# Kernel optimization log

Hardware: AMD Instinct MI355X
Metric: run time of the kernel (lower is better)

The kernel has to match this reference:

```python
import jax, jax.numpy as jnp
import numpy as np

DIM, DEPTH, HEADS, DHEAD, FF = 768, 6, 12, 64, 3072


def layer_norm(x, g, b, eps=1e-5):
    m = jnp.mean(x, axis=-1, keepdims=True)
    v = jnp.mean((x - m) ** 2, axis=-1, keepdims=True)
    return (x - m) * jax.lax.rsqrt(v + eps) * g + b


def setup_inputs() -> dict:
    key = jax.random.key(0)
    ks = jax.random.split(key, 8)
    s = 0.02
    inp = {
        "x": jax.random.normal(ks[0], (2, 2048, DIM), jnp.float32),
        "mask": jnp.ones((2, 2048), dtype=bool),
        "ln1_g": jnp.ones((DEPTH, DIM)), "ln1_b": jnp.zeros((DEPTH, DIM)),
        "w_qkv": jax.random.normal(ks[1], (DEPTH, DIM, 3 * HEADS * DHEAD)) * s,
        "w_out": jax.random.normal(ks[2], (DEPTH, HEADS * DHEAD, DIM)) * s,
        "b_out": jnp.zeros((DEPTH, DIM)),
        "ln2_g": jnp.ones((DEPTH, DIM)), "ln2_b": jnp.zeros((DEPTH, DIM)),
        "w_ff1": jax.random.normal(ks[3], (DEPTH, DIM, FF)) * s,
        "b_ff1": jnp.zeros((DEPTH, FF)),
        "w_ff2": jax.random.normal(ks[4], (DEPTH, FF, DIM)) * s,
        "b_ff2": jnp.zeros((DEPTH, DIM)),
        "lnf_g": jnp.ones((DIM,)), "lnf_b": jnp.zeros((DIM,)),
    }
    return inp


def reference(x, mask, ln1_g, ln1_b, w_qkv, w_out, b_out, ln2_g, ln2_b,
              w_ff1, b_ff1, w_ff2, b_ff2, lnf_g, lnf_b):
    scale = DHEAD ** -0.5
    b, n, _ = x.shape
    neg = -jnp.finfo(x.dtype).max
    mask4 = mask[:, None, None, :]  # b 1 1 j
    for l in range(DEPTH):
        # --- attention (pre-norm) ---
        h = layer_norm(x, ln1_g[l], ln1_b[l])
        qkv = h @ w_qkv[l]                           # [b, n, 3*h*d]
        q, k, v = jnp.split(qkv, 3, axis=-1)
        q = q.reshape(b, n, HEADS, DHEAD).transpose(0, 2, 1, 3)
        k = k.reshape(b, n, HEADS, DHEAD).transpose(0, 2, 1, 3)
        v = v.reshape(b, n, HEADS, DHEAD).transpose(0, 2, 1, 3)
        sim = jnp.einsum('bhid,bhjd->bhij', q, k) * scale
        sim = jnp.where(mask4, sim, neg)
        attn = jax.nn.softmax(sim, axis=-1)
        o = jnp.einsum('bhij,bhjd->bhid', attn, v)
        o = o.transpose(0, 2, 1, 3).reshape(b, n, HEADS * DHEAD)
        x = o @ w_out[l] + b_out[l] + x
        # --- feedforward (pre-norm) ---
        h = layer_norm(x, ln2_g[l], ln2_b[l])
        h = jax.nn.gelu(h @ w_ff1[l] + b_ff1[l], approximate=False)
        x = h @ w_ff2[l] + b_ff2[l] + x
    return layer_norm(x, lnf_g, lnf_b)
```

## Files before the change

kernel.cpp:

```cpp
#include <hip/hip_runtime.h>
#include <hip/hip_bf16.h>

typedef __attribute__((ext_vector_type(8))) short bf16x8;
typedef __attribute__((ext_vector_type(4))) float f32x4;
typedef __attribute__((ext_vector_type(16))) float f32x16;

#define DIMM 768
#define SEQ 2048
#define NBATCH 2
#define MTOT 4096
#define NHEAD 12
#define FFD 3072

static __device__ __forceinline__ unsigned short f2bfbits(float f) {
  __hip_bfloat16 h = __float2bfloat16(f);
  return __builtin_bit_cast(unsigned short, h);
}
static __device__ __forceinline__ float bf2f(short u) {
  unsigned bits = ((unsigned)(unsigned short)u) << 16;
  return __builtin_bit_cast(float, bits);
}
static __device__ __forceinline__ unsigned packbf2(float lo, float hi) {
  return (unsigned)f2bfbits(lo) | ((unsigned)f2bfbits(hi) << 16);
}
static __device__ __forceinline__ float fexp2(float x) {
  float r; asm("v_exp_f32 %0, %1" : "=v"(r) : "v"(x)); return r;
}

__global__ __launch_bounds__(256) void wconv_all(const float* __restrict__ wq,
                                                 const float* __restrict__ wo,
                                                 const float* __restrict__ wf1,
                                                 const float* __restrict__ wf2,
                                                 __hip_bfloat16* __restrict__ oq,
                                                 __hip_bfloat16* __restrict__ oo,
                                                 __hip_bfloat16* __restrict__ of1,
                                                 __hip_bfloat16* __restrict__ of2) {
  __shared__ float tile[32][33];
  int id = blockIdx.x;
  const float* in; __hip_bfloat16* out; int R, C;
  if (id < 1728)      { in = wq;  out = oq;  R = 768;  C = 2304; }
  else if (id < 2304) { id -= 1728; in = wo;  out = oo;  R = 768;  C = 768; }
  else if (id < 4608) { id -= 2304; in = wf1; out = of1; R = 768;  C = 3072; }
  else                { id -= 4608; in = wf2; out = of2; R = 3072; C = 768; }
  int tc = C >> 5;
  int rb = (id / tc) * 32, cb = (id % tc) * 32;
  int t = threadIdx.x;
  int r = t >> 3, c4 = (t & 7) << 2;
  float4 v = *(const float4*)(in + (size_t)(rb + r) * C + cb + c4);
  tile[r][c4] = v.x; tile[r][c4 + 1] = v.y; tile[r][c4 + 2] = v.z; tile[r][c4 + 3] = v.w;
  __syncthreads();
  ushort4 u;
  u.x = f2bfbits(tile[c4][r]);
  u.y = f2bfbits(tile[c4 + 1][r]);
  u.z = f2bfbits(tile[c4 + 2][r]);
  u.w = f2bfbits(tile[c4 + 3][r]);
  *(ushort4*)((unsigned short*)out + (size_t)(cb + r) * R + rb + c4) = u;
}

template<bool OUT_BF16>
__global__ __launch_bounds__(192) void ln_kernel(const float* __restrict__ x,
                                                 const float* __restrict__ g,
                                                 const float* __restrict__ b,
                                                 void* __restrict__ out) {
  int row = blockIdx.x;
  int tid = threadIdx.x;
  const float* xr = x + (size_t)row * DIMM;
  float4 v = *(const float4*)(xr + tid * 4);
  float s = v.x + v.y + v.z + v.w;
  float s2 = v.x * v.x + v.y * v.y + v.z * v.z + v.w * v.w;
  #pragma unroll
  for (int off = 32; off >= 1; off >>= 1) {
    s += __shfl_xor(s, off);
    s2 += __shfl_xor(s2, off);
  }
  __shared__ float red[6];
  int wv = tid >> 6;
  if ((tid & 63) == 0) { red[wv] = s; red[3 + wv] = s2; }
  __syncthreads();
  s = red[0] + red[1] + red[2];
  s2 = red[3] + red[4] + red[5];
  float mean = s * (1.f / DIMM);
  float var = fmaxf(s2 * (1.f / DIMM) - mean * mean, 0.f);
  float rs = rsqrtf(var + 1e-5f);
  float4 gv = *(const float4*)(g + tid * 4);
  float4 bv = *(const float4*)(b + tid * 4);
  float o0 = (v.x - mean) * rs * gv.x + bv.x;
  float o1 = (v.y - mean) * rs * gv.y + bv.y;
  float o2 = (v.z - mean) * rs * gv.z + bv.z;
  float o3 = (v.w - mean) * rs * gv.w + bv.w;
  if (OUT_BF16) {
    ushort4 u;
    u.x = f2bfbits(o0); u.y = f2bfbits(o1); u.z = f2bfbits(o2); u.w = f2bfbits(o3);
    *(ushort4*)((unsigned short*)out + (size_t)row * DIMM + tid * 4) = u;
  } else {
    float4 o;
    o.x = o0; o.y = o1; o.z = o2; o.w = o3;
    *(float4*)((float*)out + (size_t)row * DIMM + tid * 4) = o;
  }
}

enum { EPI_BF16 = 0, EPI_GELU_BF16 = 1, EPI_RES_F32 = 2, EPI_QKV = 3 };

template<int EPI, int BM, int BN>
__global__ __launch_bounds__(256) void gemm_nt(const __hip_bfloat16* __restrict__ A,
                                               const __hip_bfloat16* __restrict__ Bt,
                                               const float* __restrict__ bias,
                                               const float* resid,
                                               void* Cout, __hip_bfloat16* vtout,
                                               int M, int N, int K) {
  constexpr int FM = BM / 32, FN = BN / 32;
  constexpr int CHA = BM / 32, CHB = BN / 32;
  __shared__ __hip_bfloat16 Alds[2][BM * 64];
  __shared__ __hip_bfloat16 Blds[2][BN * 64];
  const int tid = threadIdx.x;
  const int lane = tid & 63, wid = tid >> 6;
  const int wm = wid >> 1, wn = wid & 1;
  const int lo = lane & 15, hi = lane >> 4;
  const int m0 = blockIdx.x * BM, n0 = blockIdx.y * BN;
  const int srow = lane >> 3, scol = (lane & 7) * 8;

  auto stage = [&](int buf, int k0) {
    #pragma unroll
    for (int c = 0; c < CHA; ++c) {
      int ch = wid * CHA + c;
      int row = ch * 8 + srow;
      const __hip_bfloat16* ga = A + (size_t)(m0 + row) * K + k0 + scol;
      __builtin_amdgcn_global_load_lds((const __attribute__((address_space(1))) void*)ga,
                                       (__attribute__((address_space(3))) void*)(&Alds[buf][0] + ch * 512), 16, 0, 0);
    }
    #pragma unroll
    for (int c = 0; c < CHB; ++c) {
      int ch = wid * CHB + c;
      int row = ch * 8 + srow;
      const __hip_bfloat16* gb = Bt + (size_t)(n0 + row) * K + k0 + scol;
      __builtin_amdgcn_global_load_lds((const __attribute__((address_space(1))) void*)gb,
                                       (__attribute__((address_space(3))) void*)(&Blds[buf][0] + ch * 512), 16, 0, 0);
    }
  };

  f32x4 acc[FM][FN] = {};
  stage(0, 0);
  __syncthreads();
  int cur = 0;
  for (int k0 = 0; k0 < K; k0 += 64) {
    if (k0 + 64 < K) stage(cur ^ 1, k0 + 64);
    const __hip_bfloat16* Ab = &Alds[cur][0];
    const __hip_bfloat16* Bb = &Blds[cur][0];
    #pragma unroll
    for (int kb = 0; kb < 64; kb += 32) {
      bf16x8 af[FM], bfr[FN];
      #pragma unroll
      for (int m = 0; m < FM; ++m)
        af[m] = *(const bf16x8*)(Ab + (wm * (BM / 2) + m * 16 + lo) * 64 + kb + hi * 8);
      #pragma unroll
      for (int n = 0; n < FN; ++n)
        bfr[n] = *(const bf16x8*)(Bb + (wn * (BN / 2) + n * 16 + lo) * 64 + kb + hi * 8);
      #pragma unroll
      for (int m = 0; m < FM; ++m)
        #pragma unroll
        for (int n = 0; n < FN; ++n)
          acc[m][n] = __builtin_amdgcn_mfma_f32_16x16x32_bf16(af[m], bfr[n], acc[m][n], 0, 0, 0);
    }
    __syncthreads();
    cur ^= 1;
  }
  if (EPI == EPI_QKV && n0 >= 1536) {
    #pragma unroll
    for (int m = 0; m < FM; ++m) {
      int rowb = m0 + wm * (BM / 2) + m * 16 + hi * 4;
      int b = rowb >> 11, q = rowb & 2047;
      #pragma unroll
      for (int n = 0; n < FN; ++n) {
        int col = n0 + wn * (BN / 2) + n * 16 + lo;
        int dg = col - 1536;
        int hh = dg >> 6, d = dg & 63;
        ushort4 u;
        u.x = f2bfbits(acc[m][n][0]);
        u.y = f2bfbits(acc[m][n][1]);
        u.z = f2bfbits(acc[m][n][2]);
        u.w = f2bfbits(acc[m][n][3]);
        *(ushort4*)((unsigned short*)vtout + (((size_t)(b * NHEAD + hh) * 64 + d) << 11) + q) = u;
      }
    }
    return;
  }
  #pragma unroll
  for (int m = 0; m < FM; ++m) {
    int rowb = m0 + wm * (BM / 2) + m * 16 + hi * 4;
    #pragma unroll
    for (int n = 0; n < FN; ++n) {
      int col = n0 + wn * (BN / 2) + n * 16 + lo;
      float bv = (EPI == EPI_BF16 || EPI == EPI_QKV) ? 0.f : bias[col];
      #pragma unroll
      for (int i = 0; i < 4; ++i) {
        float v = acc[m][n][i] + bv;
        size_t idx = (size_t)(rowb + i) * N + col;
        if (EPI == EPI_GELU_BF16) {
          v = 0.5f * v * (1.f + erff(v * 0.70710678118654752f));
          ((unsigned short*)Cout)[idx] = f2bfbits(v);
        } else if (EPI == EPI_RES_F32) {
          ((float*)Cout)[idx] = v + resid[idx];
        } else {
          ((unsigned short*)Cout)[idx] = f2bfbits(v);
        }
      }
    }
  }
}

__global__ __launch_bounds__(256) void attn_kernel(const __hip_bfloat16* __restrict__ qkv,
                                                   const __hip_bfloat16* __restrict__ vt,
                                                   __hip_bfloat16* __restrict__ opart,
                                                   float2* __restrict__ mlbuf) {
  __shared__ __hip_bfloat16 Klds[2][64 * 64];
  __shared__ __hip_bfloat16 Vlds[2][64 * 64];
  const int tid = threadIdx.x;
  const int lane = tid & 63, wid = tid >> 6;
  const int q32 = lane & 31, h5 = lane >> 5;
  const int bh = blockIdx.y, bb = bh / NHEAD, h = bh % NHEAD;
  const int z = blockIdx.z;
  const int kvbase = z * (SEQ / 2);
  const int q0 = blockIdx.x * 128 + wid * 32;
  const size_t pitch = 3 * DIMM;

  bf16x8 qf[4];
  {
    const __hip_bfloat16* Qp = qkv + (size_t)(bb * SEQ + q0 + q32) * pitch + h * 64;
    #pragma unroll
    for (int t4 = 0; t4 < 4; ++t4) {
      bf16x8 r = *(const bf16x8*)(Qp + t4 * 16 + h5 * 8);
      #pragma unroll
      for (int j = 0; j < 8; ++j)
        r[j] = (short)f2bfbits(bf2f(r[j]) * 0.18033688011112042f);
      qf[t4] = r;
    }
  }

  const int sk = tid >> 2;
  const int sc = tid & 3;
  const __hip_bfloat16* Kg = qkv + (size_t)bb * SEQ * pitch + DIMM + h * 64;
  const __hip_bfloat16* Vg = vt + (size_t)bh * 64 * SEQ;
  const int kswz0 = 8 * (sc ^ (sk & 7));
  const int kswz1 = 8 * ((sc + 4) ^ (sk & 7));

  bf16x8 k0r, k1r, v0r, v1r;
  {
    const __hip_bfloat16* kg = Kg + (size_t)(kvbase + sk) * pitch;
    k0r = *(const bf16x8*)(kg + sc * 8);
    k1r = *(const bf16x8*)(kg + sc * 8 + 32);
    const __hip_bfloat16* vg = Vg + (size_t)sk * SEQ + kvbase;
    v0r = *(const bf16x8*)(vg + sc * 8);
    v1r = *(const bf16x8*)(vg + sc * 8 + 32);
  }

  f32x16 accO0 = {}, accO1 = {};
  float m_run = -1e30f, l_run = 0.f;

  const int NT = (SEQ / 2) / 64;
  for (int t = 0; t < NT; ++t) {
    __hip_bfloat16* Kb = Klds[t & 1];
    __hip_bfloat16* Vb = Vlds[t & 1];
    *(bf16x8*)(Kb + sk * 64 + kswz0) = k0r;
    *(bf16x8*)(Kb + sk * 64 + kswz1) = k1r;
    *(bf16x8*)(Vb + sk * 64 + kswz0) = v0r;
    *(bf16x8*)(Vb + sk * 64 + kswz1) = v1r;
    __syncthreads();
    if (t + 1 < NT) {
      int kv0 = kvbase + (t + 1) * 64;
      const __hip_bfloat16* kg = Kg + (size_t)(kv0 + sk) * pitch;
      k0r = *(const bf16x8*)(kg + sc * 8);
      k1r = *(const bf16x8*)(kg + sc * 8 + 32);
      const __hip_bfloat16* vg = Vg + (size_t)sk * SEQ + kv0;
      v0r = *(const bf16x8*)(vg + sc * 8);
      v1r = *(const bf16x8*)(vg + sc * 8 + 32);
    }

    #pragma unroll
    for (int sub = 0; sub < 2; ++sub) {
      const int krow = sub * 32 + q32;
      f32x16 sacc = {};
      __builtin_amdgcn_s_setprio(1);
      #pragma unroll
      for (int t4 = 0; t4 < 4; ++t4) {
        bf16x8 kf = *(const bf16x8*)(Kb + krow * 64 + 8 * ((2 * t4 + h5) ^ (krow & 7)));
        sacc = __builtin_amdgcn_mfma_f32_32x32x16_bf16(kf, qf[t4], sacc, 0, 0, 0);
      }
      __builtin_amdgcn_s_setprio(0);
      float red[8];
      #pragma unroll
      for (int r = 0; r < 8; ++r) red[r] = fmaxf(sacc[r], sacc[r + 8]);
      #pragma unroll
      for (int r = 0; r < 4; ++r) red[r] = fmaxf(red[r], red[r + 4]);
      red[0] = fmaxf(red[0], red[2]); red[1] = fmaxf(red[1], red[3]);
      float vmax = fmaxf(red[0], red[1]);
      vmax = fmaxf(vmax, __shfl_xor(vmax, 32));
      if (!__all(vmax <= m_run + 8.f)) {
        float mnew = fmaxf(m_run, vmax);
        float alpha = fexp2(m_run - mnew);
        #pragma unroll
        for (int r = 0; r < 16; ++r) { accO0[r] *= alpha; accO1[r] *= alpha; }
        l_run *= alpha;
        m_run = mnew;
      }
      float p[16];
      #pragma unroll
      for (int r = 0; r < 16; ++r) p[r] = fexp2(sacc[r] - m_run);
      float sr[8];
      #pragma unroll
      for (int r = 0; r < 8; ++r) sr[r] = p[r] + p[r + 8];
      #pragma unroll
      for (int r = 0; r < 4; ++r) sr[r] = sr[r] + sr[r + 4];
      float lsum = (sr[0] + sr[1]) + (sr[2] + sr[3]);
      lsum += __shfl_xor(lsum, 32);
      l_run += lsum;
      unsigned c0 = packbf2(p[0], p[1]),   c1 = packbf2(p[2], p[3]);
      unsigned c2 = packbf2(p[4], p[5]),   c3 = packbf2(p[6], p[7]);
      unsigned c4 = packbf2(p[8], p[9]),   c5 = packbf2(p[10], p[11]);
      unsigned c6 = packbf2(p[12], p[13]), c7 = packbf2(p[14], p[15]);
      auto r20 = __builtin_amdgcn_permlane32_swap((int)c2, (int)c0, false, false);
      auto r31 = __builtin_amdgcn_permlane32_swap((int)c3, (int)c1, false, false);
      auto r64 = __builtin_amdgcn_permlane32_swap((int)c6, (int)c4, false, false);
      auto r75 = __builtin_amdgcn_permlane32_swap((int)c7, (int)c5, false, false);
      int4 pw0i = { r20[1], r31[1], r20[0], r31[0] };
      int4 pw1i = { r64[1], r75[1], r64[0], r75[0] };
      bf16x8 pf0 = __builtin_bit_cast(bf16x8, pw0i);
      bf16x8 pf1 = __builtin_bit_cast(bf16x8, pw1i);
      const int d0 = q32, d1 = 32 + q32;
      bf16x8 a00 = *(const bf16x8*)(Vb + d0 * 64 + 8 * ((sub * 4 + 0 + h5) ^ (d0 & 7)));
      bf16x8 a01 = *(const bf16x8*)(Vb + d0 * 64 + 8 * ((sub * 4 + 2 + h5) ^ (d0 & 7)));
      bf16x8 a10 = *(const bf16x8*)(Vb + d1 * 64 + 8 * ((sub * 4 + 0 + h5) ^ (d1 & 7)));
      bf16x8 a11 = *(const bf16x8*)(Vb + d1 * 64 + 8 * ((sub * 4 + 2 + h5) ^ (d1 & 7)));
      __builtin_amdgcn_s_setprio(1);
      accO0 = __builtin_amdgcn_mfma_f32_32x32x16_bf16(a00, pf0, accO0, 0, 0, 0);
      accO0 = __builtin_amdgcn_mfma_f32_32x32x16_bf16(a01, pf1, accO0, 0, 0, 0);
      accO1 = __builtin_amdgcn_mfma_f32_32x32x16_bf16(a10, pf0, accO1, 0, 0, 0);
      accO1 = __builtin_amdgcn_mfma_f32_32x32x16_bf16(a11, pf1, accO1, 0, 0, 0);
      __builtin_amdgcn_s_setprio(0);
    }
  }

  float linv = 1.f / l_run;
  unsigned short* orow = (unsigned short*)opart + (size_t)z * MTOT * DIMM +
                         (size_t)(bb * SEQ + q0 + q32) * DIMM + h * 64;
  #pragma unroll
  for (int g = 0; g < 4; ++g) {
    ushort4 u0, u1;
    u0.x = f2bfbits(accO0[g * 4 + 0] * linv);
    u0.y = f2bfbits(accO0[g * 4 + 1] * linv);
    u0.z = f2bfbits(accO0[g * 4 + 2] * linv);
    u0.w = f2bfbits(accO0[g * 4 + 3] * linv);
    *(ushort4*)(orow + g * 8 + h5 * 4) = u0;
    u1.x = f2bfbits(accO1[g * 4 + 0] * linv);
    u1.y = f2bfbits(accO1[g * 4 + 1] * linv);
    u1.z = f2bfbits(accO1[g * 4 + 2] * linv);
    u1.w = f2bfbits(accO1[g * 4 + 3] * linv);
    *(ushort4*)(orow + 32 + g * 8 + h5 * 4) = u1;
  }
  if (h5 == 0)
    mlbuf[((size_t)(z * 24 + bh) << 11) + q0 + q32] = make_float2(m_run, l_run);
}

__global__ __launch_bounds__(256) void attn_combine(const __hip_bfloat16* __restrict__ opart,
                                                    const float2* __restrict__ ml,
                                                    __hip_bfloat16* __restrict__ out) {
  int g = blockIdx.x * 256 + threadIdx.x;
  int row = g / 96;
  int cw = g - row * 96;
  int h = cw >> 3;
  int b = row >> 11, q = row & 2047;
  int bh = b * NHEAD + h;
  float2 ml0 = ml[((size_t)bh << 11) + q];
  float2 ml1 = ml[((size_t)(24 + bh) << 11) + q];
  float m = fmaxf(ml0.x, ml1.x);
  float w0 = fexp2(ml0.x - m) * ml0.y;
  float w1 = fexp2(ml1.x - m) * ml1.y;
  float inv = 1.f / (w0 + w1);
  w0 *= inv; w1 *= inv;
  size_t off = (size_t)row * DIMM + cw * 8;
  bf16x8 o0 = *(const bf16x8*)((const unsigned short*)opart + off);
  bf16x8 o1 = *(const bf16x8*)((const unsigned short*)opart + (size_t)MTOT * DIMM + off);
  bf16x8 r;
  #pragma unroll
  for (int j = 0; j < 8; ++j)
    r[j] = (short)f2bfbits(w0 * bf2f(o0[j]) + w1 * bf2f(o1[j]));
  *(bf16x8*)((unsigned short*)out + off) = r;
}

extern "C" void kernel_launch(void* const* d_in, const int* in_sizes, int n_in,
                              void* d_out, int out_size, void* d_ws, size_t ws_size,
                              hipStream_t stream) {
  const float* x_in  = (const float*)d_in[0];
  const float* ln1_g = (const float*)d_in[2];
  const float* ln1_b = (const float*)d_in[3];
  const float* w_qkv = (const float*)d_in[4];
  const float* w_out = (const float*)d_in[5];
  const float* b_out = (const float*)d_in[6];
  const float* ln2_g = (const float*)d_in[7];
  const float* ln2_b = (const float*)d_in[8];
  const float* w_ff1 = (const float*)d_in[9];
  const float* b_ff1 = (const float*)d_in[10];
  const float* w_ff2 = (const float*)d_in[11];
  const float* b_ff2 = (const float*)d_in[12];
  const float* lnf_g = (const float*)d_in[13];
  const float* lnf_b = (const float*)d_in[14];

  const size_t OFF_X    = 0;
  const size_t OFF_H    = 12582912;
  const size_t OFF_QKV  = OFF_H + 6291456;
  const size_t OFF_AO   = OFF_QKV + 18874368;
  const size_t OFF_FFH  = OFF_AO + 6291456;
  const size_t OFF_WQKV = OFF_FFH + 25165824;
  const size_t OFF_WOUT = OFF_WQKV + 3538944;
  const size_t OFF_WFF1 = OFF_WOUT + 1179648;
  const size_t OFF_WFF2 = OFF_WFF1 + 4718592;
  const size_t NEED     = OFF_WFF2 + 4718592;
  if (ws_size < NEED) return;

  char* ws = (char*)d_ws;
  float* x              = (float*)(ws + OFF_X);
  __hip_bfloat16* h     = (__hip_bfloat16*)(ws + OFF_H);
  float2* mlbuf         = (float2*)(ws + OFF_H);
  __hip_bfloat16* qkvb  = (__hip_bfloat16*)(ws + OFF_QKV);
  __hip_bfloat16* ao    = (__hip_bfloat16*)(ws + OFF_AO);
  __hip_bfloat16* ffh   = (__hip_bfloat16*)(ws + OFF_FFH);
  __hip_bfloat16* vtb   = (__hip_bfloat16*)(ws + OFF_FFH);
  __hip_bfloat16* opart = (__hip_bfloat16*)(ws + OFF_FFH + 6291456);
  __hip_bfloat16* wqkvt = (__hip_bfloat16*)(ws + OFF_WQKV);
  __hip_bfloat16* woutt = (__hip_bfloat16*)(ws + OFF_WOUT);
  __hip_bfloat16* wff1t = (__hip_bfloat16*)(ws + OFF_WFF1);
  __hip_bfloat16* wff2t = (__hip_bfloat16*)(ws + OFF_WFF2);

  hipMemcpyAsync(x, x_in, (size_t)MTOT * DIMM * 4, hipMemcpyDeviceToDevice, stream);

  for (int l = 0; l < 6; ++l) {
    wconv_all<<<6912, 256, 0, stream>>>(
        w_qkv + (size_t)l * DIMM * 3 * DIMM,
        w_out + (size_t)l * DIMM * DIMM,
        w_ff1 + (size_t)l * DIMM * FFD,
        w_ff2 + (size_t)l * FFD * DIMM,
        wqkvt, woutt, wff1t, wff2t);

    ln_kernel<true><<<MTOT, 192, 0, stream>>>(x, ln1_g + l * DIMM, ln1_b + l * DIMM, h);
    gemm_nt<EPI_QKV, 128, 96><<<dim3(MTOT / 128, (3 * DIMM) / 96), 256, 0, stream>>>(
        h, wqkvt, nullptr, nullptr, qkvb, vtb, MTOT, 3 * DIMM, DIMM);
    attn_kernel<<<dim3(SEQ / 128, NBATCH * NHEAD, 2), 256, 0, stream>>>(qkvb, vtb, opart, mlbuf);
    attn_combine<<<(MTOT * DIMM / 8) / 256, 256, 0, stream>>>(opart, mlbuf, ao);
    gemm_nt<EPI_RES_F32, 64, 64><<<dim3(MTOT / 64, DIMM / 64), 256, 0, stream>>>(
        ao, woutt, b_out + l * DIMM, x, x, nullptr, MTOT, DIMM, DIMM);
    ln_kernel<true><<<MTOT, 192, 0, stream>>>(x, ln2_g + l * DIMM, ln2_b + l * DIMM, h);
    gemm_nt<EPI_GELU_BF16, 128, 128><<<dim3(MTOT / 128, FFD / 128), 256, 0, stream>>>(
        h, wff1t, b_ff1 + (size_t)l * FFD, nullptr, ffh, nullptr, MTOT, FFD, DIMM);
    gemm_nt<EPI_RES_F32, 64, 64><<<dim3(MTOT / 64, DIMM / 64), 256, 0, stream>>>(
        ffh, wff2t, b_ff2 + l * DIMM, x, x, nullptr, MTOT, DIMM, FFD);
  }
  ln_kernel<false><<<MTOT, 192, 0, stream>>>(x, lnf_g, lnf_b, d_out);
}
```

Baseline: 1.329 ms.

## Halve GEMM K-tile to 32 and XOR-swizzle LDS layout to avoid bank conflicts

Changes the GEMM staging tile from 64 to 32 along K and applies an XOR swizzle on 16-byte column chunks, keyed on row, both when loading global data into LDS and when reading fragments. The swizzle targets LDS bank conflicts on fragment reads with a row stride of 64 bf16 elements. Halving the K tile halves LDS use, which may raise occupancy, but doubles the number of loop iterations and __syncthreads barriers per GEMM.

```diff
diff --git a/kernel.cpp b/kernel.cpp
--- a/kernel.cpp
+++ b/kernel.cpp
@@ -109,32 +109,39 @@
                                                void* Cout, __hip_bfloat16* vtout,
                                                int M, int N, int K) {
   constexpr int FM = BM / 32, FN = BN / 32;
-  constexpr int CHA = BM / 32, CHB = BN / 32;
-  __shared__ __hip_bfloat16 Alds[2][BM * 64];
-  __shared__ __hip_bfloat16 Blds[2][BN * 64];
+  constexpr int TLA = BM / 16, TLB = BN / 16;
+  __shared__ __hip_bfloat16 Alds[2][BM * 32];
+  __shared__ __hip_bfloat16 Blds[2][BN * 32];
   const int tid = threadIdx.x;
   const int lane = tid & 63, wid = tid >> 6;
   const int wm = wid >> 1, wn = wid & 1;
   const int lo = lane & 15, hi = lane >> 4;
   const int m0 = blockIdx.x * BM, n0 = blockIdx.y * BN;
-  const int srow = lane >> 3, scol = (lane & 7) * 8;
+  const int lrow = lane >> 2;
+  const int lcc = lane & 3;
 
   auto stage = [&](int buf, int k0) {
     #pragma unroll
-    for (int c = 0; c < CHA; ++c) {
-      int ch = wid * CHA + c;
-      int row = ch * 8 + srow;
-      const __hip_bfloat16* ga = A + (size_t)(m0 + row) * K + k0 + scol;
-      __builtin_amdgcn_global_load_lds((const __attribute__((address_space(1))) void*)ga,
-                                       (__attribute__((address_space(3))) void*)(&Alds[buf][0] + ch * 512), 16, 0, 0);
-    }
-    #pragma unroll
-    for (int c = 0; c < CHB; ++c) {
-      int ch = wid * CHB + c;
-      int row = ch * 8 + srow;
-      const __hip_bfloat16* gb = Bt + (size_t)(n0 + row) * K + k0 + scol;
-      __builtin_amdgcn_global_load_lds((const __attribute__((address_space(1))) void*)gb,
-                                       (__attribute__((address_space(3))) void*)(&Blds[buf][0] + ch * 512), 16, 0, 0);
+    for (int c = 0; c < (TLA + 3) / 4; ++c) {
+      int ld = c * 4 + wid;
+      if (TLA % 4 == 0 || ld < TLA) {
+        int row = ld * 16 + lrow;
+        int cc = lcc ^ (row & 3);
+        const __hip_bfloat16* ga = A + (size_t)(m0 + row) * K + k0 + cc * 8;
+        __builtin_amdgcn_global_load_lds((const __attribute__((address_space(1))) void*)ga,
+                                         (__attribute__((address_space(3))) void*)(&Alds[buf][0] + ld * 512), 16, 0, 0);
+      }
+    }
+    #pragma unroll
+    for (int c = 0; c < (TLB + 3) / 4; ++c) {
+      int ld = c * 4 + wid;
+      if (TLB % 4 == 0 || ld < TLB) {
+        int row = ld * 16 + lrow;
+        int cc = lcc ^ (row & 3);
+        const __hip_bfloat16* gb = Bt + (size_t)(n0 + row) * K + k0 + cc * 8;
+        __builtin_amdgcn_global_load_lds((const __attribute__((address_space(1))) void*)gb,
+                                         (__attribute__((address_space(3))) void*)(&Blds[buf][0] + ld * 512), 16, 0, 0);
+      }
     }
   };
 
@@ -142,25 +149,26 @@
   stage(0, 0);
   __syncthreads();
   int cur = 0;
-  for (int k0 = 0; k0 < K; k0 += 64) {
-    if (k0 + 64 < K) stage(cur ^ 1, k0 + 64);
+  for (int k0 = 0; k0 < K; k0 += 32) {
+    if (k0 + 32 < K) stage(cur ^ 1, k0 + 32);
     const __hip_bfloat16* Ab = &Alds[cur][0];
     const __hip_bfloat16* Bb = &Blds[cur][0];
-    #pragma unroll
-    for (int kb = 0; kb < 64; kb += 32) {
-      bf16x8 af[FM], bfr[FN];
-      #pragma unroll
-      for (int m = 0; m < FM; ++m)
-        af[m] = *(const bf16x8*)(Ab + (wm * (BM / 2) + m * 16 + lo) * 64 + kb + hi * 8);
+    bf16x8 af[FM], bfr[FN];
+    #pragma unroll
+    for (int m = 0; m < FM; ++m) {
+      int row = wm * (BM / 2) + m * 16 + lo;
+      af[m] = *(const bf16x8*)(Ab + row * 32 + 8 * (hi ^ (row & 3)));
+    }
+    #pragma unroll
+    for (int n = 0; n < FN; ++n) {
+      int row = wn * (BN / 2) + n * 16 + lo;
+      bfr[n] = *(const bf16x8*)(Bb + row * 32 + 8 * (hi ^ (row & 3)));
+    }
+    #pragma unroll
+    for (int m = 0; m < FM; ++m)
       #pragma unroll
       for (int n = 0; n < FN; ++n)
-        bfr[n] = *(const bf16x8*)(Bb + (wn * (BN / 2) + n * 16 + lo) * 64 + kb + hi * 8);
-      #pragma unroll
-      for (int m = 0; m < FM; ++m)
-        #pragma unroll
-        for (int n = 0; n < FN; ++n)
-          acc[m][n] = __builtin_amdgcn_mfma_f32_16x16x32_bf16(af[m], bfr[n], acc[m][n], 0, 0, 0);
-    }
+        acc[m][n] = __builtin_amdgcn_mfma_f32_16x16x32_bf16(af[m], bfr[n], acc[m][n], 0, 0, 0);
     __syncthreads();
     cur ^= 1;
   }
```

Result: faster. 1.142 ms (-14.1%).
